# Optimization experiments

Hardware: AMD Instinct MI355X
Metric: run time of the kernel (lower is better)

The kernel has to match this reference:

```python
import jax, jax.numpy as jnp
import numpy as np

IN_DIM = 512

def setup_inputs() -> dict:
    key = jax.random.key(0)
    ks = jax.random.split(key, 7)
    s = 1.0 / np.sqrt(IN_DIM)
    x = jax.random.normal(ks[0], (8, 2048, IN_DIM), dtype=jnp.float32)
    Wq = jax.random.uniform(ks[1], (IN_DIM, IN_DIM), jnp.float32, -s, s)
    bq = jax.random.uniform(ks[2], (IN_DIM,), jnp.float32, -s, s)
    Wk = jax.random.uniform(ks[3], (IN_DIM, IN_DIM), jnp.float32, -s, s)
    bk = jax.random.uniform(ks[4], (IN_DIM,), jnp.float32, -s, s)
    Wv = jax.random.uniform(ks[5], (IN_DIM, IN_DIM), jnp.float32, -s, s)
    bv = jax.random.uniform(ks[6], (IN_DIM,), jnp.float32, -s, s)
    return {"x": x, "Wq": Wq, "bq": bq, "Wk": Wk, "bk": bk, "Wv": Wv, "bv": bv}

def reference(x, Wq, bq, Wk, bk, Wv, bv):
    # Q,K,V projections: torch Linear is x @ W.T + b; Wq here is [out,in]
    q = jnp.einsum('bsc,dc->bsd', x, Wq) + bq
    k = jnp.einsum('bsc,dc->bsd', x, Wk) + bk
    v = jnp.einsum('bsc,dc->bsd', x, Wv) + bv
    energy = jnp.einsum('bqd,bkd->bqk', q, k)  # no scaling, matches source
    attention = jax.nn.softmax(energy, axis=-1)
    out = jnp.einsum('bqk,bkd->bqd', attention, v)
    return out
```

## Files before the change

### kernel.cpp

```cpp
#include <hip/hip_runtime.h>

typedef unsigned short u16;
typedef _Float16 f16;

using half8   = __attribute__((ext_vector_type(8))) _Float16;
using f32x4   = __attribute__((ext_vector_type(4))) float;
using ushort8 = __attribute__((ext_vector_type(8))) unsigned short;
using us4     = __attribute__((ext_vector_type(4))) unsigned short;
using float4v = __attribute__((ext_vector_type(4))) float;

#define B_  8
#define S_  2048
#define D_  512

__device__ __forceinline__ u16 f2h(float f) {
  f16 h = (f16)f;
  u16 u;
  __builtin_memcpy(&u, &h, 2);
  return u;
}

__device__ __forceinline__ float h2f(u16 h) {
  f16 x;
  __builtin_memcpy(&x, &h, 2);
  return (float)x;
}

__device__ __forceinline__ void stage16(const void* g, void* l) {
  __builtin_amdgcn_global_load_lds((const __attribute__((address_space(1))) void*)g,
                                   (__attribute__((address_space(3))) void*)l,
                                   16, 0, 0);
}

__device__ __forceinline__ void xcd_remap(int& bx, int& by, int& bz) {
  const int lin = ((int)blockIdx.z * (int)gridDim.y + (int)blockIdx.y) * (int)gridDim.x
                  + (int)blockIdx.x;
  const int nwg = (int)gridDim.x * (int)gridDim.y * (int)gridDim.z;
  const int swz = (lin & 7) * (nwg >> 3) + (lin >> 3);
  bx = swz % (int)gridDim.x;
  const int tmp = swz / (int)gridDim.x;
  by = tmp % (int)gridDim.y;
  bz = tmp / (int)gridDim.y;
}

template<int M_REP>
__device__ __forceinline__ void core8p(const u16* __restrict__ A,
                                       const u16* __restrict__ B,
                                       int K, int m0, int n0,
                                       u16* lds, f32x4 acc[M_REP][4]) {
  constexpr int M2   = M_REP / 2;
  constexpr int BM   = M_REP * 32;
  constexpr int AIS  = BM * 32;
  constexpr int BOFF = BM * 64;
  constexpr int BUFE = BM * 64 + 16384;
  constexpr int ASL  = BM / 128;
  constexpr int L    = 2 * ASL + 4;
  constexpr int QSRA = (BM == 256) ? 32 : 16;

  const int tid  = threadIdx.x;
  const int lane = tid & 63;
  const int wave = tid >> 6;
  const int wr = wave >> 2, wc = wave & 3;
  const int fr = lane & 15, fgrp = lane >> 4;

  int    dstA[2][ASL];  size_t gA[2][ASL];
  int    dstB[2][2];    size_t gB[2][2];
  #pragma unroll
  for (int q = 0; q < 2; ++q) {
    #pragma unroll
    for (int s = 0; s < ASL; ++s) {
      int ks, jr;
      if constexpr (ASL == 2) { ks = s; jr = wave * 8; }
      else                    { ks = wave >> 2; jr = (wave & 3) * 8; }
      const int R   = (jr / QSRA) * (2 * QSRA) + q * QSRA + (jr % QSRA);
      const int dst = ks * AIS + R * 64;
      dstA[q][s] = dst;
      const int e   = dst + lane * 8;
      const int ks2 = e / AIS, le = e - ks2 * AIS;
      const int RR  = le >> 6;
      const int s0  = ((le >> 3) & 7) ^ (RR & 7);
      gA[q][s] = (size_t)(m0 + 2 * RR + (s0 >> 2)) * K + ks2 * 32 + (s0 & 3) * 8;
    }
    #pragma unroll
    for (int s = 0; s < 2; ++s) {
      const int jr  = wave * 8;
      const int R   = (jr / 16) * 32 + q * 16 + (jr % 16);
      const int dst = BOFF + s * 8192 + R * 64;
      dstB[q][s] = dst;
      const int e   = dst - BOFF + lane * 8;
      const int ks2 = e / 8192, le = e - ks2 * 8192;
      const int RR  = le >> 6;
      const int s0  = ((le >> 3) & 7) ^ (RR & 7);
      gB[q][s] = (size_t)(n0 + 2 * RR + (s0 >> 2)) * K + ks2 * 32 + (s0 & 3) * 8;
    }
  }

  int offA[2][M2][2], offB[2][2][2];
  #pragma unroll
  for (int mh = 0; mh < 2; ++mh)
    #pragma unroll
    for (int m = 0; m < M2; ++m)
      #pragma unroll
      for (int ks = 0; ks < 2; ++ks) {
        const int ra = wr * (M_REP * 16) + (mh * M2 + m) * 16 + fr;
        const int Ra = ra >> 1;
        offA[mh][m][ks] = (ks * AIS + Ra * 64) * 2 +
                          (((((ra & 1) << 2) | fgrp) ^ (Ra & 7)) << 4);
      }
  #pragma unroll
  for (int nh = 0; nh < 2; ++nh)
    #pragma unroll
    for (int n = 0; n < 2; ++n)
      #pragma unroll
      for (int ks = 0; ks < 2; ++ks) {
        const int rb = wc * 64 + (nh * 2 + n) * 16 + fr;
        const int Rb = rb >> 1;
        offB[nh][n][ks] = (BOFF + ks * 8192 + Rb * 64) * 2 +
                          (((((rb & 1) << 2) | fgrp) ^ (Rb & 7)) << 4);
      }

  const f32x4 vzero = {0.f, 0.f, 0.f, 0.f};
  #pragma unroll
  for (int m = 0; m < M_REP; ++m)
    #pragma unroll
    for (int n = 0; n < 4; ++n)
      acc[m][n] = vzero;

  const int NT = K >> 6;

  auto stageA = [&](int q, int tt) {
    u16* bb = lds + (tt & 1) * BUFE;
    #pragma unroll
    for (int s = 0; s < ASL; ++s)
      stage16(A + gA[q][s] + (size_t)tt * 64, bb + dstA[q][s]);
  };
  auto stageB = [&](int q, int tt) {
    u16* bb = lds + (tt & 1) * BUFE;
    #pragma unroll
    for (int s = 0; s < 2; ++s)
      stage16(B + gB[q][s] + (size_t)tt * 64, bb + dstB[q][s]);
  };

  stageA(0, 0); stageB(0, 0); stageB(1, 0); stageA(1, 0);
  stageA(0, 1); stageB(0, 1); stageB(1, 1); stageA(1, 1);

  half8 a[M2][2], blo[2][2], bhi[2][2];

#define MFMA_Q(MH, BB, NB)                                                       \
  __builtin_amdgcn_s_setprio(1);                                                 \
  _Pragma("unroll")                                                              \
  for (int m = 0; m < M2; ++m)                                                   \
    _Pragma("unroll")                                                            \
    for (int n = 0; n < 2; ++n)                                                  \
      _Pragma("unroll")                                                          \
      for (int ks = 0; ks < 2; ++ks)                                             \
        acc[(MH) * M2 + m][(NB) + n] = __builtin_amdgcn_mfma_f32_16x16x32_f16(   \
            a[m][ks], BB[n][ks], acc[(MH) * M2 + m][(NB) + n], 0, 0, 0);         \
  __builtin_amdgcn_s_setprio(0);

  for (int t = 0; t < NT; ++t) {
    const char* rb_ = (const char*)(lds + (t & 1) * BUFE);
    const int tt = t + 2;
    const bool st = (tt < NT);

    if (t == NT - 1) asm volatile("s_waitcnt vmcnt(0)\n\ts_barrier" ::: "memory");
    else if constexpr (L == 8) asm volatile("s_waitcnt vmcnt(8)\n\ts_barrier" ::: "memory");
    else                       asm volatile("s_waitcnt vmcnt(6)\n\ts_barrier" ::: "memory");
    #pragma unroll
    for (int m = 0; m < M2; ++m)
      #pragma unroll
      for (int ks = 0; ks < 2; ++ks)
        a[m][ks] = *(const half8*)(rb_ + offA[0][m][ks]);
    #pragma unroll
    for (int n = 0; n < 2; ++n)
      #pragma unroll
      for (int ks = 0; ks < 2; ++ks)
        blo[n][ks] = *(const half8*)(rb_ + offB[0][n][ks]);
    MFMA_Q(0, blo, 0)
    asm volatile("s_barrier" ::: "memory");

    #pragma unroll
    for (int n = 0; n < 2; ++n)
      #pragma unroll
      for (int ks = 0; ks < 2; ++ks)
        bhi[n][ks] = *(const half8*)(rb_ + offB[1][n][ks]);
    if (st) { stageA(0, tt); stageB(0, tt); }
    asm volatile("s_barrier" ::: "memory");
    MFMA_Q(0, bhi, 2)
    asm volatile("s_barrier" ::: "memory");

    #pragma unroll
    for (int m = 0; m < M2; ++m)
      #pragma unroll
      for (int ks = 0; ks < 2; ++ks)
        a[m][ks] = *(const half8*)(rb_ + offA[1][m][ks]);
    if (st) stageB(1, tt);
    asm volatile("s_barrier" ::: "memory");
    MFMA_Q(1, bhi, 2)
    asm volatile("s_barrier" ::: "memory");

    if (st) stageA(1, tt);
    asm volatile("s_barrier" ::: "memory");
    MFMA_Q(1, blo, 0)
    asm volatile("s_barrier" ::: "memory");
  }
#undef MFMA_Q
}

__global__ __launch_bounds__(512, 1) void proj_kernel(
    const u16* __restrict__ xh, const u16* __restrict__ Wh,
    const float* __restrict__ bq, const float* __restrict__ bk, const float* __restrict__ bv,
    u16* __restrict__ Qb, u16* __restrict__ Kb, u16* __restrict__ Vt) {
  __shared__ __align__(16) u16 lds[2 * (128 * 64 + 16384)];
  int bx, by, bz;
  xcd_remap(bx, by, bz);
  const int z  = bz;
  const int m0 = by * 128;
  const int n0 = bx * 256;
  const u16* W = Wh + (size_t)z * D_ * D_;
  const float* bias = (z == 0) ? bq : (z == 1) ? bk : bv;
  f32x4 acc[4][4];
  core8p<4>(xh, W, D_, m0, n0, lds, acc);

  const int lane = threadIdx.x & 63;
  const int wave = threadIdx.x >> 6;
  const int wr = wave >> 2, wc = wave & 3;
  #pragma unroll
  for (int m = 0; m < 4; ++m) {
    const int gr0 = m0 + wr * 64 + m * 16 + ((lane >> 4) << 2);
    #pragma unroll
    for (int n = 0; n < 4; ++n) {
      const int gc = n0 + wc * 64 + n * 16 + (lane & 15);
      const float bb = bias[gc];
      if (z < 2) {
        u16* O = z ? Kb : Qb;
        #pragma unroll
        for (int r = 0; r < 4; ++r)
          O[(size_t)(gr0 + r) * D_ + gc] = f2h(acc[m][n][r] + bb);
      } else {
        const int bidx = gr0 >> 11;
        const int s    = gr0 & 2047;
        us4 p;
        #pragma unroll
        for (int r = 0; r < 4; ++r) p[r] = f2h(acc[m][n][r] + bb);
        *(us4*)(Vt + ((size_t)bidx * D_ + gc) * S_ + s) = p;
      }
    }
  }
}

__global__ __launch_bounds__(512, 1) void qk_kernel(
    const u16* __restrict__ Qb, const u16* __restrict__ Kb, u16* __restrict__ E,
    size_t sA, size_t sE) {
  __shared__ __align__(16) u16 lds[2 * (256 * 64 + 16384)];
  int bx, by, bz;
  xcd_remap(bx, by, bz);
  const int z  = bz;
  const int m0 = by * 256;
  const int n0 = bx * 256;
  f32x4 acc[8][4];
  core8p<8>(Qb + (size_t)z * sA, Kb + (size_t)z * sA, D_, m0, n0, lds, acc);

  u16* Eb = E + (size_t)z * sE;
  const int lane = threadIdx.x & 63;
  const int wave = threadIdx.x >> 6;
  const int wr = wave >> 2, wc = wave & 3;
  #pragma unroll
  for (int m = 0; m < 8; ++m) {
    const int gr0 = m0 + wr * 128 + m * 16 + ((lane >> 4) << 2);
    #pragma unroll
    for (int n = 0; n < 4; ++n) {
      const int gc = n0 + wc * 64 + n * 16 + (lane & 15);
      #pragma unroll
      for (int r = 0; r < 4; ++r)
        Eb[(size_t)(gr0 + r) * S_ + gc] = f2h(acc[m][n][r]);
    }
  }
}

__global__ __launch_bounds__(256) void softmax_kernel(u16* __restrict__ E) {
  const int row  = blockIdx.x * 4 + (threadIdx.x >> 6);
  const int lane = threadIdx.x & 63;
  u16* R = E + (size_t)row * S_;
  float e[32];
  #pragma unroll
  for (int i = 0; i < 4; ++i) {
    ushort8 v = *(const ushort8*)(R + i * 512 + lane * 8);
    #pragma unroll
    for (int j = 0; j < 8; ++j) e[i * 8 + j] = h2f(v[j]);
  }
  float m = e[0];
  #pragma unroll
  for (int i = 1; i < 32; ++i) m = fmaxf(m, e[i]);
  for (int off = 32; off > 0; off >>= 1) m = fmaxf(m, __shfl_xor(m, off, 64));
  float s = 0.f;
  #pragma unroll
  for (int i = 0; i < 32; ++i) { e[i] = __expf(e[i] - m); s += e[i]; }
  for (int off = 32; off > 0; off >>= 1) s += __shfl_xor(s, off, 64);
  const float inv = 1.f / s;
  #pragma unroll
  for (int i = 0; i < 4; ++i) {
    ushort8 v;
    #pragma unroll
    for (int j = 0; j < 8; ++j) v[j] = f2h(e[i * 8 + j] * inv);
    *(ushort8*)(R + i * 512 + lane * 8) = v;
  }
}

__global__ __launch_bounds__(512, 1) void pv_kernel(
    const u16* __restrict__ P, const u16* __restrict__ Vt, float* __restrict__ out,
    size_t sP, size_t sV, size_t sO) {
  __shared__ __align__(16) u16 lds[2 * (128 * 64 + 16384)];
  int bx, by, bz;
  xcd_remap(bx, by, bz);
  const int z  = bz;
  const int m0 = by * 128;
  const int n0 = bx * 256;
  f32x4 acc[4][4];
  core8p<4>(P + (size_t)z * sP, Vt + (size_t)z * sV, S_, m0, n0, lds, acc);

  float* Ob = out + (size_t)z * sO;
  const int lane = threadIdx.x & 63;
  const int wave = threadIdx.x >> 6;
  const int wr = wave >> 2, wc = wave & 3;
  #pragma unroll
  for (int m = 0; m < 4; ++m) {
    const int gr0 = m0 + wr * 64 + m * 16 + ((lane >> 4) << 2);
    #pragma unroll
    for (int n = 0; n < 4; ++n) {
      const int gc = n0 + wc * 64 + n * 16 + (lane & 15);
      #pragma unroll
      for (int r = 0; r < 4; ++r)
        Ob[(size_t)(gr0 + r) * D_ + gc] = acc[m][n][r];
    }
  }
}

__global__ __launch_bounds__(256) void cvt_kernel(const float* __restrict__ in,
                                                  u16* __restrict__ out, int n8) {
  const int i = blockIdx.x * 256 + threadIdx.x;
  if (i >= n8) return;
  const float4v a = *(const float4v*)(in + (size_t)i * 8);
  const float4v b = *(const float4v*)(in + (size_t)i * 8 + 4);
  ushort8 o;
  o[0] = f2h(a[0]); o[1] = f2h(a[1]); o[2] = f2h(a[2]); o[3] = f2h(a[3]);
  o[4] = f2h(b[0]); o[5] = f2h(b[1]); o[6] = f2h(b[2]); o[7] = f2h(b[3]);
  *(ushort8*)(out + (size_t)i * 8) = o;
}

__global__ __launch_bounds__(256) void cvt3_kernel(const float* __restrict__ w0,
                                                   const float* __restrict__ w1,
                                                   const float* __restrict__ w2,
                                                   u16* __restrict__ out, int n8) {
  const int i = blockIdx.x * 256 + threadIdx.x;
  if (i >= n8) return;
  const float* in = (blockIdx.y == 0) ? w0 : (blockIdx.y == 1) ? w1 : w2;
  u16* o_ = out + (size_t)blockIdx.y * D_ * D_;
  const float4v a = *(const float4v*)(in + (size_t)i * 8);
  const float4v b = *(const float4v*)(in + (size_t)i * 8 + 4);
  ushort8 o;
  o[0] = f2h(a[0]); o[1] = f2h(a[1]); o[2] = f2h(a[2]); o[3] = f2h(a[3]);
  o[4] = f2h(b[0]); o[5] = f2h(b[1]); o[6] = f2h(b[2]); o[7] = f2h(b[3]);
  *(ushort8*)(o_ + (size_t)i * 8) = o;
}

extern "C" void kernel_launch(void* const* d_in, const int* in_sizes, int n_in,
                              void* d_out, int out_size, void* d_ws, size_t ws_size,
                              hipStream_t stream) {
  (void)in_sizes; (void)n_in; (void)out_size;
  const float* x  = (const float*)d_in[0];
  const float* Wq = (const float*)d_in[1];
  const float* bq = (const float*)d_in[2];
  const float* Wk = (const float*)d_in[3];
  const float* bk = (const float*)d_in[4];
  const float* Wv = (const float*)d_in[5];
  const float* bv = (const float*)d_in[6];
  float* out = (float*)d_out;

  char* ws = (char*)d_ws;
  size_t off = 0;
  auto alloc = [&](size_t bytes) -> char* {
    char* p = ws + off;
    off += (bytes + 255) & ~(size_t)255;
    return p;
  };
  const size_t MS = (size_t)B_ * S_;
  u16* xh = (u16*)alloc(MS * D_ * 2);
  u16* Wh = (u16*)alloc(3ull * D_ * D_ * 2);
  u16* Qb = (u16*)alloc(MS * D_ * 2);
  u16* Kb = (u16*)alloc(MS * D_ * 2);
  u16* Vt = (u16*)alloc(MS * D_ * 2);
  const size_t Efull = (size_t)B_ * S_ * S_ * 2;
  const bool full = ws_size >= off + Efull;
  u16* E = (u16*)alloc(full ? Efull : (size_t)S_ * S_ * 2);

  {
    const int n8 = (int)(MS * D_ / 8);
    cvt_kernel<<<dim3((n8 + 255) / 256), dim3(256), 0, stream>>>(x, xh, n8);
    const int w8 = D_ * D_ / 8;
    cvt3_kernel<<<dim3((w8 + 255) / 256, 3), dim3(256), 0, stream>>>(Wq, Wk, Wv, Wh, w8);
  }

  proj_kernel<<<dim3(D_ / 256, MS / 128, 3), dim3(512), 0, stream>>>(
      xh, Wh, bq, bk, bv, Qb, Kb, Vt);

  if (full) {
    qk_kernel<<<dim3(S_ / 256, S_ / 256, B_), dim3(512), 0, stream>>>(
        Qb, Kb, E, (size_t)S_ * D_, (size_t)S_ * S_);
    softmax_kernel<<<dim3(B_ * S_ / 4), dim3(256), 0, stream>>>(E);
    pv_kernel<<<dim3(D_ / 256, S_ / 128, B_), dim3(512), 0, stream>>>(
        E, Vt, out, (size_t)S_ * S_, (size_t)D_ * S_, (size_t)S_ * D_);
  } else {
    for (int b = 0; b < B_; ++b) {
      qk_kernel<<<dim3(S_ / 256, S_ / 256, 1), dim3(512), 0, stream>>>(
          Qb + (size_t)b * S_ * D_, Kb + (size_t)b * S_ * D_, E, 0, 0);
      softmax_kernel<<<dim3(S_ / 4), dim3(256), 0, stream>>>(E);
      pv_kernel<<<dim3(D_ / 256, S_ / 128, 1), dim3(512), 0, stream>>>(
          E, Vt + (size_t)b * D_ * S_, out + (size_t)b * S_ * D_, 0, 0, 0);
    }
  }
}
```

Measured before the change: 162.8 us.

## Fuse softmax stats into QK epilogue and apply exp normalization inside PV

```diff
diff --git a/kernel.cpp b/kernel.cpp
--- a/kernel.cpp
+++ b/kernel.cpp
@@ -43,11 +43,12 @@
   bz = tmp / (int)gridDim.y;
 }
 
-template<int M_REP>
+template<int M_REP, bool EXPA = false>
 __device__ __forceinline__ void core8p(const u16* __restrict__ A,
                                        const u16* __restrict__ B,
                                        int K, int m0, int n0,
-                                       u16* lds, f32x4 acc[M_REP][4]) {
+                                       u16* lds, f32x4 acc[M_REP][4],
+                                       const float2* __restrict__ mlv = nullptr) {
   constexpr int M2   = M_REP / 2;
   constexpr int BM   = M_REP * 32;
   constexpr int AIS  = BM * 32;
@@ -158,6 +159,23 @@
             a[m][ks], BB[n][ks], acc[(MH) * M2 + m][(NB) + n], 0, 0, 0);         \
   __builtin_amdgcn_s_setprio(0);
 
+#define EXP_A(MH)                                                                \
+  if constexpr (EXPA) {                                                          \
+    _Pragma("unroll")                                                            \
+    for (int m = 0; m < M2; ++m) {                                               \
+      const float mm = mlv[(MH) * M2 + m].x;                                     \
+      const float li = mlv[(MH) * M2 + m].y;                                     \
+      _Pragma("unroll")                                                          \
+      for (int ks = 0; ks < 2; ++ks) {                                           \
+        half8 h = a[m][ks];                                                      \
+        _Pragma("unroll")                                                        \
+        for (int j = 0; j < 8; ++j)                                              \
+          h[j] = (f16)(__expf((float)h[j] - mm) * li);                           \
+        a[m][ks] = h;                                                            \
+      }                                                                          \
+    }                                                                            \
+  }
+
   for (int t = 0; t < NT; ++t) {
     const char* rb_ = (const char*)(lds + (t & 1) * BUFE);
     const int tt = t + 2;
@@ -176,6 +194,7 @@
       #pragma unroll
       for (int ks = 0; ks < 2; ++ks)
         blo[n][ks] = *(const half8*)(rb_ + offB[0][n][ks]);
+    EXP_A(0)
     MFMA_Q(0, blo, 0)
     asm volatile("s_barrier" ::: "memory");
 
@@ -196,6 +215,7 @@
         a[m][ks] = *(const half8*)(rb_ + offA[1][m][ks]);
     if (st) stageB(1, tt);
     asm volatile("s_barrier" ::: "memory");
+    EXP_A(1)
     MFMA_Q(1, bhi, 2)
     asm volatile("s_barrier" ::: "memory");
 
@@ -205,6 +225,7 @@
     asm volatile("s_barrier" ::: "memory");
   }
 #undef MFMA_Q
+#undef EXP_A
 }
 
 __global__ __launch_bounds__(512, 1) void proj_kernel(
@@ -251,7 +272,7 @@
 
 __global__ __launch_bounds__(512, 1) void qk_kernel(
     const u16* __restrict__ Qb, const u16* __restrict__ Kb, u16* __restrict__ E,
-    size_t sA, size_t sE) {
+    float2* __restrict__ stat, size_t sA, size_t sE) {
   __shared__ __align__(16) u16 lds[2 * (256 * 64 + 16384)];
   int bx, by, bz;
   xcd_remap(bx, by, bz);
@@ -262,53 +283,74 @@
   core8p<8>(Qb + (size_t)z * sA, Kb + (size_t)z * sA, D_, m0, n0, lds, acc);
 
   u16* Eb = E + (size_t)z * sE;
-  const int lane = threadIdx.x & 63;
-  const int wave = threadIdx.x >> 6;
+  const int tid  = threadIdx.x;
+  const int lane = tid & 63;
+  const int wave = tid >> 6;
   const int wr = wave >> 2, wc = wave & 3;
+  const int g  = lane >> 4;
+  const int fr = lane & 15;
+  float* sf = (float*)lds;
+
   #pragma unroll
   for (int m = 0; m < 8; ++m) {
-    const int gr0 = m0 + wr * 128 + m * 16 + ((lane >> 4) << 2);
-    #pragma unroll
-    for (int n = 0; n < 4; ++n) {
-      const int gc = n0 + wc * 64 + n * 16 + (lane & 15);
-      #pragma unroll
-      for (int r = 0; r < 4; ++r)
-        Eb[(size_t)(gr0 + r) * S_ + gc] = f2h(acc[m][n][r]);
-    }
-  }
-}
-
-__global__ __launch_bounds__(256) void softmax_kernel(u16* __restrict__ E) {
-  const int row  = blockIdx.x * 4 + (threadIdx.x >> 6);
-  const int lane = threadIdx.x & 63;
-  u16* R = E + (size_t)row * S_;
-  float e[32];
-  #pragma unroll
-  for (int i = 0; i < 4; ++i) {
-    ushort8 v = *(const ushort8*)(R + i * 512 + lane * 8);
-    #pragma unroll
-    for (int j = 0; j < 8; ++j) e[i * 8 + j] = h2f(v[j]);
-  }
-  float m = e[0];
-  #pragma unroll
-  for (int i = 1; i < 32; ++i) m = fmaxf(m, e[i]);
-  for (int off = 32; off > 0; off >>= 1) m = fmaxf(m, __shfl_xor(m, off, 64));
-  float s = 0.f;
-  #pragma unroll
-  for (int i = 0; i < 32; ++i) { e[i] = __expf(e[i] - m); s += e[i]; }
-  for (int off = 32; off > 0; off >>= 1) s += __shfl_xor(s, off, 64);
-  const float inv = 1.f / s;
-  #pragma unroll
-  for (int i = 0; i < 4; ++i) {
-    ushort8 v;
-    #pragma unroll
-    for (int j = 0; j < 8; ++j) v[j] = f2h(e[i * 8 + j] * inv);
-    *(ushort8*)(R + i * 512 + lane * 8) = v;
-  }
+    const int gr0 = m0 + wr * 128 + m * 16 + (g << 2);
+    #pragma unroll
+    for (int r = 0; r < 4; ++r) {
+      float v[4], vm = -3.0e38f;
+      #pragma unroll
+      for (int n = 0; n < 4; ++n) {
+        const int gc = n0 + wc * 64 + n * 16 + fr;
+        const u16 hb = f2h(acc[m][n][r]);
+        Eb[(size_t)(gr0 + r) * S_ + gc] = hb;
+        v[n] = h2f(hb);
+        vm = fmaxf(vm, v[n]);
+      }
+      #pragma unroll
+      for (int o = 1; o < 16; o <<= 1) vm = fmaxf(vm, __shfl_xor(vm, o, 64));
+      float ls = 0.f;
+      #pragma unroll
+      for (int n = 0; n < 4; ++n) ls += __expf(v[n] - vm);
+      #pragma unroll
+      for (int o = 1; o < 16; o <<= 1) ls += __shfl_xor(ls, o, 64);
+      if (fr == 0) {
+        const int lr = wr * 128 + m * 16 + g * 4 + r;
+        sf[(lr * 4 + wc) * 2 + 0] = vm;
+        sf[(lr * 4 + wc) * 2 + 1] = ls;
+      }
+    }
+  }
+  __syncthreads();
+  if (tid < 256) {
+    float mm[4], ll[4], m4 = -3.0e38f;
+    #pragma unroll
+    for (int j = 0; j < 4; ++j) {
+      mm[j] = sf[(tid * 4 + j) * 2 + 0];
+      ll[j] = sf[(tid * 4 + j) * 2 + 1];
+      m4 = fmaxf(m4, mm[j]);
+    }
+    float l = 0.f;
+    #pragma unroll
+    for (int j = 0; j < 4; ++j) l += ll[j] * __expf(mm[j] - m4);
+    stat[((size_t)z * S_ + (m0 + tid)) * 8 + bx] = make_float2(m4, l);
+  }
+}
+
+__global__ __launch_bounds__(256) void merge_kernel(const float2* __restrict__ st,
+                                                    float2* __restrict__ ml) {
+  const int i = blockIdx.x * 256 + threadIdx.x;
+  float2 s[8];
+  float m = -3.0e38f;
+  #pragma unroll
+  for (int j = 0; j < 8; ++j) { s[j] = st[(size_t)i * 8 + j]; m = fmaxf(m, s[j].x); }
+  float l = 0.f;
+  #pragma unroll
+  for (int j = 0; j < 8; ++j) l += s[j].y * __expf(s[j].x - m);
+  ml[i] = make_float2(m, 1.f / l);
 }
 
 __global__ __launch_bounds__(512, 1) void pv_kernel(
-    const u16* __restrict__ P, const u16* __restrict__ Vt, float* __restrict__ out,
+    const u16* __restrict__ Eb, const u16* __restrict__ Vt,
+    const float2* __restrict__ ml, float* __restrict__ out,
     size_t sP, size_t sV, size_t sO) {
   __shared__ __align__(16) u16 lds[2 * (128 * 64 + 16384)];
   int bx, by, bz;
@@ -316,13 +358,21 @@
   const int z  = bz;
   const int m0 = by * 128;
   const int n0 = bx * 256;
-  f32x4 acc[4][4];
-  core8p<4>(P + (size_t)z * sP, Vt + (size_t)z * sV, S_, m0, n0, lds, acc);
-
-  float* Ob = out + (size_t)z * sO;
   const int lane = threadIdx.x & 63;
   const int wave = threadIdx.x >> 6;
   const int wr = wave >> 2, wc = wave & 3;
+
+  float2 mlv[4];
+  #pragma unroll
+  for (int mh = 0; mh < 2; ++mh)
+    #pragma unroll
+    for (int m = 0; m < 2; ++m)
+      mlv[mh * 2 + m] = ml[(size_t)z * S_ + m0 + wr * 64 + (mh * 2 + m) * 16 + (lane & 15)];
+
+  f32x4 acc[4][4];
+  core8p<4, true>(Eb + (size_t)z * sP, Vt + (size_t)z * sV, S_, m0, n0, lds, acc, mlv);
+
+  float* Ob = out + (size_t)z * sO;
   #pragma unroll
   for (int m = 0; m < 4; ++m) {
     const int gr0 = m0 + wr * 64 + m * 16 + ((lane >> 4) << 2);
@@ -385,11 +435,13 @@
     return p;
   };
   const size_t MS = (size_t)B_ * S_;
-  u16* xh = (u16*)alloc(MS * D_ * 2);
-  u16* Wh = (u16*)alloc(3ull * D_ * D_ * 2);
-  u16* Qb = (u16*)alloc(MS * D_ * 2);
-  u16* Kb = (u16*)alloc(MS * D_ * 2);
-  u16* Vt = (u16*)alloc(MS * D_ * 2);
+  u16*    xh    = (u16*)alloc(MS * D_ * 2);
+  u16*    Wh    = (u16*)alloc(3ull * D_ * D_ * 2);
+  u16*    Qb    = (u16*)alloc(MS * D_ * 2);
+  u16*    Kb    = (u16*)alloc(MS * D_ * 2);
+  u16*    Vt    = (u16*)alloc(MS * D_ * 2);
+  float2* stats = (float2*)alloc(MS * 8 * sizeof(float2));
+  float2* ML    = (float2*)alloc(MS * sizeof(float2));
   const size_t Efull = (size_t)B_ * S_ * S_ * 2;
   const bool full = ws_size >= off + Efull;
   u16* E = (u16*)alloc(full ? Efull : (size_t)S_ * S_ * 2);
@@ -406,17 +458,17 @@
 
   if (full) {
     qk_kernel<<<dim3(S_ / 256, S_ / 256, B_), dim3(512), 0, stream>>>(
-        Qb, Kb, E, (size_t)S_ * D_, (size_t)S_ * S_);
-    softmax_kernel<<<dim3(B_ * S_ / 4), dim3(256), 0, stream>>>(E);
+        Qb, Kb, E, stats, (size_t)S_ * D_, (size_t)S_ * S_);
+    merge_kernel<<<dim3((int)(MS / 256)), dim3(256), 0, stream>>>(stats, ML);
     pv_kernel<<<dim3(D_ / 256, S_ / 128, B_), dim3(512), 0, stream>>>(
-        E, Vt, out, (size_t)S_ * S_, (size_t)D_ * S_, (size_t)S_ * D_);
+        E, Vt, ML, out, (size_t)S_ * S_, (size_t)D_ * S_, (size_t)S_ * D_);
   } else {
     for (int b = 0; b < B_; ++b) {
       qk_kernel<<<dim3(S_ / 256, S_ / 256, 1), dim3(512), 0, stream>>>(
-          Qb + (size_t)b * S_ * D_, Kb + (size_t)b * S_ * D_, E, 0, 0);
-      softmax_kernel<<<dim3(S_ / 4), dim3(256), 0, stream>>>(E);
+          Qb + (size_t)b * S_ * D_, Kb + (size_t)b * S_ * D_, E, stats, 0, 0);
+      merge_kernel<<<dim3(S_ / 256), dim3(256), 0, stream>>>(stats, ML);
       pv_kernel<<<dim3(D_ / 256, S_ / 128, 1), dim3(512), 0, stream>>>(
-          E, Vt + (size_t)b * D_ * S_, out + (size_t)b * S_ * D_, 0, 0, 0);
-    }
-  }
-}
+          E, Vt + (size_t)b * D_ * S_, ML, out + (size_t)b * S_ * D_, 0, 0, 0);
+    }
+  }
+}
```

After: 210.1 us. 29.0% more time.

## Replace projection GEMM core with 128x128 triple-buffered tile kernel

Applied to the files above, without the earlier changes.

```diff
diff --git a/kernel.cpp b/kernel.cpp
--- a/kernel.cpp
+++ b/kernel.cpp
@@ -41,6 +41,90 @@
   const int tmp = swz / (int)gridDim.x;
   by = tmp % (int)gridDim.y;
   bz = tmp / (int)gridDim.y;
+}
+
+__device__ __forceinline__ void gemm128(const u16* __restrict__ A, const u16* __restrict__ B,
+                                        int K, int m0, int n0,
+                                        u16* lds, f32x4 acc[4][4]) {
+  constexpr int TILE_ELEMS = 4096;
+  constexpr int BUF_ELEMS  = 8192;
+  const int tid  = threadIdx.x;
+  const int lane = tid & 63;
+  const int wave = tid >> 6;
+  const int wr = wave >> 1, wc = wave & 1;
+  const int fr   = lane & 15;
+  const int fgrp = lane >> 4;
+
+  int sr[2], sc[2];
+  #pragma unroll
+  for (int s = 0; s < 2; ++s) {
+    const int p    = tid * 16 + s * 4096;
+    const int R    = p >> 7;
+    const int slot = (p >> 4) & 7;
+    const int s0   = slot ^ (R & 7);
+    sr[s] = 2 * R + (s0 >> 2);
+    sc[s] = (s0 & 3) * 8;
+  }
+
+  int offA[4], offB[4];
+  #pragma unroll
+  for (int m = 0; m < 4; ++m) {
+    const int ra = wr * 64 + m * 16 + fr;
+    const int Ra = ra >> 1;
+    offA[m] = Ra * 128 + (((((ra & 1) << 2) | fgrp) ^ (Ra & 7)) << 4);
+    const int rb = wc * 64 + m * 16 + fr;
+    const int Rb = rb >> 1;
+    offB[m] = Rb * 128 + (((((rb & 1) << 2) | fgrp) ^ (Rb & 7)) << 4);
+  }
+
+  const f32x4 vzero = {0.f, 0.f, 0.f, 0.f};
+  #pragma unroll
+  for (int m = 0; m < 4; ++m)
+    #pragma unroll
+    for (int n = 0; n < 4; ++n)
+      acc[m][n] = vzero;
+
+  const int T = K / 32;
+
+  auto STAGE = [&](int t, u16* buf) {
+    #pragma unroll
+    for (int s = 0; s < 2; ++s) {
+      stage16(A + (size_t)(m0 + sr[s]) * K + t * 32 + sc[s],
+              buf + s * 2048 + wave * 512);
+      stage16(B + (size_t)(n0 + sr[s]) * K + t * 32 + sc[s],
+              buf + TILE_ELEMS + s * 2048 + wave * 512);
+    }
+  };
+
+  STAGE(0, lds);
+  STAGE(1, lds + BUF_ELEMS);
+
+  int r = 0;
+  for (int u = 0; u < T; ++u) {
+    if (u + 1 < T) {
+      asm volatile("s_waitcnt vmcnt(4)\n\ts_barrier" ::: "memory");
+    } else {
+      asm volatile("s_waitcnt vmcnt(0)\n\ts_barrier" ::: "memory");
+    }
+    const u16* buf = lds + r * BUF_ELEMS;
+    half8 a[4], b[4];
+    #pragma unroll
+    for (int m = 0; m < 4; ++m)
+      a[m] = *(const half8*)((const char*)buf + offA[m]);
+    #pragma unroll
+    for (int n = 0; n < 4; ++n)
+      b[n] = *(const half8*)((const char*)(buf + TILE_ELEMS) + offB[n]);
+    if (u + 2 < T)
+      STAGE(u + 2, lds + (r == 0 ? 2 : r - 1) * BUF_ELEMS);
+    __builtin_amdgcn_s_setprio(1);
+    #pragma unroll
+    for (int m = 0; m < 4; ++m)
+      #pragma unroll
+      for (int n = 0; n < 4; ++n)
+        acc[m][n] = __builtin_amdgcn_mfma_f32_16x16x32_f16(a[m], b[n], acc[m][n], 0, 0, 0);
+    __builtin_amdgcn_s_setprio(0);
+    r = (r == 2) ? 0 : r + 1;
+  }
 }
 
 template<int M_REP>
@@ -207,24 +291,24 @@
 #undef MFMA_Q
 }
 
-__global__ __launch_bounds__(512, 1) void proj_kernel(
+__global__ __launch_bounds__(256) void proj_kernel(
     const u16* __restrict__ xh, const u16* __restrict__ Wh,
     const float* __restrict__ bq, const float* __restrict__ bk, const float* __restrict__ bv,
     u16* __restrict__ Qb, u16* __restrict__ Kb, u16* __restrict__ Vt) {
-  __shared__ __align__(16) u16 lds[2 * (128 * 64 + 16384)];
+  __shared__ __align__(16) u16 lds[3 * 8192];
   int bx, by, bz;
   xcd_remap(bx, by, bz);
   const int z  = bz;
   const int m0 = by * 128;
-  const int n0 = bx * 256;
+  const int n0 = bx * 128;
   const u16* W = Wh + (size_t)z * D_ * D_;
   const float* bias = (z == 0) ? bq : (z == 1) ? bk : bv;
   f32x4 acc[4][4];
-  core8p<4>(xh, W, D_, m0, n0, lds, acc);
+  gemm128(xh, W, D_, m0, n0, lds, acc);
 
   const int lane = threadIdx.x & 63;
   const int wave = threadIdx.x >> 6;
-  const int wr = wave >> 2, wc = wave & 3;
+  const int wr = wave >> 1, wc = wave & 1;
   #pragma unroll
   for (int m = 0; m < 4; ++m) {
     const int gr0 = m0 + wr * 64 + m * 16 + ((lane >> 4) << 2);
@@ -401,7 +485,7 @@
     cvt3_kernel<<<dim3((w8 + 255) / 256, 3), dim3(256), 0, stream>>>(Wq, Wk, Wv, Wh, w8);
   }
 
-  proj_kernel<<<dim3(D_ / 256, MS / 128, 3), dim3(512), 0, stream>>>(
+  proj_kernel<<<dim3(D_ / 128, MS / 128, 3), dim3(256), 0, stream>>>(
       xh, Wh, bq, bk, bv, Qb, Kb, Vt);
 
   if (full) {
```

Measured after the change: 156.9 us. 3.6% less time.
